# Performance work log

Hardware: AMD Instinct MI355X
Metric: run time of the kernel (lower is better)

The kernel has to match this reference:

```python
import jax, jax.numpy as jnp
import numpy as np

N = 50000          # nodes
E = 800000         # edges (avg in-degree 16)
NFEAT, F = 128, 64 # input feat, hidden width (outfeat = outd_1 = outd_2 = 64)
ALPHA = 0.2        # leaky relu slope
AVG_LIN = 16.0             # sum(bin*hist)/N for deg histogram (all deg 16)
AVG_LOG = float(np.log(17.0))  # sum(log(bin+1)*hist)/N


def setup_inputs():
    key = jax.random.key(0)
    ks = jax.random.split(key, 16)
    g = lambda i, shp, s: (jax.random.normal(ks[i], shp, jnp.float32) * s)
    return {
        "x": g(0, (N, NFEAT), 1.0),
        "adj": jnp.zeros((1,), jnp.float32),
        "edge_index": jax.random.randint(ks[1], (2, E), 0, N, dtype=jnp.int32),
        "W0": g(2, (NFEAT, F), NFEAT ** -0.5), "b0": jnp.zeros((F,), jnp.float32),
        "c1_pre_W": g(3, (2 * F, F), (2 * F) ** -0.5), "c1_pre_b": jnp.zeros((F,), jnp.float32),
        "c1_post_W": g(4, (5 * F, F), (5 * F) ** -0.5), "c1_post_b": jnp.zeros((F,), jnp.float32),
        "c1_lin_W": g(5, (F, F), F ** -0.5), "c1_lin_b": jnp.zeros((F,), jnp.float32),
        "c2_pre_W": g(6, (2 * F, F), (2 * F) ** -0.5), "c2_pre_b": jnp.zeros((F,), jnp.float32),
        "c2_post_W": g(7, (5 * F, F), (5 * F) ** -0.5), "c2_post_b": jnp.zeros((F,), jnp.float32),
        "c2_lin_W": g(8, (F, F), F ** -0.5), "c2_lin_b": jnp.zeros((F,), jnp.float32),
        "W2": g(9, (F, 1), F ** -0.5), "b2": jnp.zeros((1,), jnp.float32),
    }


def pna_conv(x, src, dst, pre_W, pre_b, post_W, post_b, lin_W, lin_b):
    # message: pre_nn(cat[x_i, x_j]) per edge  (x_i = target, x_j = source)
    h = jnp.concatenate([x[dst], x[src]], axis=-1) @ pre_W + pre_b  # [E, F]
    cnt = jax.ops.segment_sum(jnp.ones((h.shape[0],), h.dtype), dst, num_segments=N)
    deg = jnp.clip(cnt, 1.0)                                        # [N]
    mean = jax.ops.segment_sum(h, dst, num_segments=N) / deg[:, None]
    mx = jax.ops.segment_max(h, dst, num_segments=N)
    mx = jnp.where(cnt[:, None] > 0, mx, 0.0)                       # empty segs -> 0
    agg = jnp.concatenate([mean, mx], axis=-1)                      # [N, 2F]
    att = agg * (AVG_LOG / jnp.log(deg + 1.0))[:, None]             # attenuation scaler
    lin = agg * (deg / AVG_LIN)[:, None]                            # linear scaler
    out = jnp.concatenate([x, att, lin], axis=-1)                   # [N, 5F]
    out = out @ post_W + post_b
    return out @ lin_W + lin_b


def reference(x, adj, edge_index, W0, b0,
              c1_pre_W, c1_pre_b, c1_post_W, c1_post_b, c1_lin_W, c1_lin_b,
              c2_pre_W, c2_pre_b, c2_post_W, c2_post_b, c2_lin_W, c2_lin_b,
              W2, b2):
    src, dst = edge_index[0], edge_index[1]
    h = jax.nn.leaky_relu(x @ W0 + b0, negative_slope=ALPHA)  # dropout = id (eval)
    h = jax.nn.relu(pna_conv(h, src, dst, c1_pre_W, c1_pre_b, c1_post_W, c1_post_b, c1_lin_W, c1_lin_b))
    h = jax.nn.relu(pna_conv(h, src, dst, c2_pre_W, c2_pre_b, c2_post_W, c2_post_b, c2_lin_W, c2_lin_b))
    return h @ W2 + b2  # [N, 1]
```

## Files before the change

### kernel.cpp

```cpp
#include <hip/hip_runtime.h>
#include <hip/hip_bf16.h>

typedef __hip_bfloat16 bf16;
typedef unsigned short u16;
typedef unsigned int u32;
typedef __attribute__((ext_vector_type(8))) short short8;
typedef __attribute__((ext_vector_type(4))) float f32x4;

static constexpr float AVG_LOG_C = 2.8332133440562162f;
#define BCAP 1024
#define CHUNK 4096
#define PREP_TOTAL (8192 * 3 + 20480 * 2 + 64 * 6 + 1)

__device__ __forceinline__ u32 f2bf_bits(float f) {
    u32 u = __float_as_uint(f);
    return (u + 0x7fffu + ((u >> 16) & 1u)) >> 16;
}
__device__ __forceinline__ float bf2f(u16 b) {
    return __uint_as_float(((u32)b) << 16);
}

__global__ __launch_bounds__(1024) void detect_zero_kernel(
    const u32* __restrict__ xwords, int* __restrict__ flag,
    int* __restrict__ bcnt, int nb) {
    if (blockIdx.x == 0) {
        int tid = threadIdx.x;
        if (tid < 64) {
            int good = 0;
            for (int i = tid; i < 2048; i += 64) {
                u32 lo = xwords[i] & 0xffffu;
                float v = __uint_as_float(lo << 16);
                float a = fabsf(v);
                if (v == 0.0f || (a >= 1e-3f && a <= 100.0f)) good++;
            }
            for (int off = 32; off; off >>= 1) good += __shfl_xor(good, off, 64);
            if (tid == 0) *flag = (2 * good > 2048) ? 1 : 0;
        }
    } else {
        int i = (blockIdx.x - 1) * 1024 + threadIdx.x;
        if (i < nb) bcnt[i] = 0;
    }
}

__global__ __launch_bounds__(1024) void prep_scatter_kernel(
    const int* __restrict__ srcs, const int* __restrict__ dsts,
    int* __restrict__ bcnt, u32* __restrict__ bstage, int e, int nb,
    const void* __restrict__ W0r,  const void* __restrict__ b0r,
    const void* __restrict__ pre1r, const void* __restrict__ preb1r,
    const void* __restrict__ post1r, const void* __restrict__ postb1r,
    const void* __restrict__ lin1r, const void* __restrict__ linb1r,
    const void* __restrict__ pre2r, const void* __restrict__ preb2r,
    const void* __restrict__ post2r, const void* __restrict__ postb2r,
    const void* __restrict__ lin2r, const void* __restrict__ linb2r,
    const void* __restrict__ W2r,  const void* __restrict__ b2r,
    u16* __restrict__ W0p, u16* __restrict__ pre1p, u16* __restrict__ pre2p,
    u16* __restrict__ wf1p, u16* __restrict__ wf2p,
    float* __restrict__ bfo1, float* __restrict__ bfo2,
    float* __restrict__ preb1f, float* __restrict__ preb2f,
    float* __restrict__ b0f, float* __restrict__ W2f, float* __restrict__ b2f,
    const int* __restrict__ flag) {
    __shared__ int lhist[2048];
    __shared__ int lbase[2048];
    int tid = threadIdx.x;
    int scatB = (e + CHUNK - 1) / CHUNK;
    if ((int)blockIdx.x < scatB) {
        int cbase = blockIdx.x * CHUNK;
        for (int b = tid; b < nb; b += 1024) lhist[b] = 0;
        __syncthreads();
#pragma unroll
        for (int i = 0; i < CHUNK; i += 1024) {
            int e0 = cbase + i + tid;
            if (e0 < e) atomicAdd(&lhist[dsts[e0] >> 5], 1);
        }
        __syncthreads();
        for (int b = tid; b < nb; b += 1024) {
            int c = lhist[b];
            lbase[b] = c ? atomicAdd(&bcnt[b], c) : 0;
            lhist[b] = 0;
        }
        __syncthreads();
#pragma unroll
        for (int i = 0; i < CHUNK; i += 1024) {
            int e0 = cbase + i + tid;
            if (e0 < e) {
                int d = dsts[e0];
                int b = d >> 5;
                int pos = lbase[b] + atomicAdd(&lhist[b], 1);
                if (pos < BCAP)
                    bstage[(size_t)b * BCAP + pos] = (u32)srcs[e0] | ((u32)(d & 31) << 17);
            }
        }
        return;
    }
    int idx = ((int)blockIdx.x - scatB) * 1024 + tid;
    bool isbf = (*flag) != 0;
    auto ld = [&](const void* p, int i) -> float {
        return isbf ? bf2f(((const u16*)p)[i]) : ((const float*)p)[i];
    };
    if (idx < 8192) {
        int j = idx & 7, l = (idx >> 3) & 63, tt = idx >> 9;
        int c = tt & 3, s = tt >> 2;
        int kk = s * 32 + (l >> 4) * 8 + j;
        int col = c * 16 + (l & 15);
        W0p[idx] = (u16)f2bf_bits(ld(W0r, kk * 64 + col));
        return;
    }
    idx -= 8192;
    for (int which = 0; which < 2; ++which) {
        if (idx < 8192) {
            const void* src = which ? pre2r : pre1r;
            u16* dst = which ? pre2p : pre1p;
            int j = idx & 7, l = (idx >> 3) & 63, tt = idx >> 9;
            int c = tt & 7, s = tt >> 3;
            int kk = s * 32 + (l >> 4) * 8 + j;
            int col = c * 16 + (l & 15);
            float v = (col < 64) ? ld(src, kk * 64 + col)
                                 : ld(src, (64 + kk) * 64 + (col - 64));
            dst[idx] = (u16)f2bf_bits(v);
            return;
        }
        idx -= 8192;
    }
    for (int which = 0; which < 2; ++which) {
        if (idx < 20480) {
            const void* postW = which ? post2r : post1r;
            const void* linW  = which ? lin2r  : lin1r;
            u16* dst = which ? wf2p : wf1p;
            int j = idx & 7, l = (idx >> 3) & 63, tt = idx >> 9;
            int c = tt & 3, s = tt >> 2;
            int kk = s * 32 + (l >> 4) * 8 + j;
            int col = c * 16 + (l & 15);
            float a = 0.f;
            for (int k = 0; k < 64; ++k)
                a = fmaf(ld(postW, kk * 64 + k), ld(linW, k * 64 + col), a);
            dst[idx] = (u16)f2bf_bits(a);
            return;
        }
        idx -= 20480;
    }
    for (int which = 0; which < 2; ++which) {
        if (idx < 64) {
            const void* postb = which ? postb2r : postb1r;
            const void* linW  = which ? lin2r : lin1r;
            const void* linb  = which ? linb2r : linb1r;
            float* dst = which ? bfo2 : bfo1;
            float a = ld(linb, idx);
            for (int k = 0; k < 64; ++k)
                a = fmaf(ld(postb, k), ld(linW, k * 64 + idx), a);
            dst[idx] = a;
            return;
        }
        idx -= 64;
    }
    if (idx < 64) { preb1f[idx] = ld(preb1r, idx); return; }
    idx -= 64;
    if (idx < 64) { preb2f[idx] = ld(preb2r, idx); return; }
    idx -= 64;
    if (idx < 64) { b0f[idx] = ld(b0r, idx); return; }
    idx -= 64;
    if (idx < 64) { W2f[idx] = ld(W2r, idx); return; }
    idx -= 64;
    if (idx < 1) { b2f[0] = ld(b2r, 0); }
}

__global__ __launch_bounds__(512, 6) void gemm_x_pq_kernel(
    const void* __restrict__ xraw, const u16* __restrict__ W0p,
    const float* __restrict__ b0f, const u16* __restrict__ pre1p,
    u16* __restrict__ hA, u16* __restrict__ PQ,
    const int* __restrict__ flag, int n) {
    __shared__ __align__(16) u16 xsh[32 * 136];
    __shared__ __align__(16) u16 hsh[32 * 72];
    int tid = threadIdx.x;
    int wave = __builtin_amdgcn_readfirstlane(tid >> 6);
    int lane = tid & 63;
    int blockbase = blockIdx.x * 32;
    bool isbf = (*flag) != 0;
    {
        int row = tid >> 4;
        int cg = (tid & 15) * 8;
        int grow = blockbase + row;
        short8 v = short8{0, 0, 0, 0, 0, 0, 0, 0};
        if (grow < n) {
            if (isbf) {
                v = *(const short8*)((const u16*)xraw + (size_t)grow * 128 + cg);
            } else {
                const float* xf = (const float*)xraw + (size_t)grow * 128 + cg;
                f32x4 a0 = *(const f32x4*)xf;
                f32x4 a1 = *(const f32x4*)(xf + 4);
#pragma unroll
                for (int j = 0; j < 4; ++j) {
                    v[j]     = (short)f2bf_bits(a0[j]);
                    v[4 + j] = (short)f2bf_bits(a1[j]);
                }
            }
        }
        *(short8*)&xsh[row * 136 + cg] = v;
    }
    __syncthreads();
    int rt = wave & 1, ct = wave >> 1;
    int arl = rt * 16 + (lane & 15);
    int koff = (lane >> 4) * 8;
    f32x4 acc = f32x4{0.f, 0.f, 0.f, 0.f};
#pragma unroll
    for (int s = 0; s < 4; ++s) {
        short8 a = *(const short8*)&xsh[arl * 136 + s * 32 + koff];
        short8 b = *(const short8*)(W0p + ((size_t)(s * 4 + ct) * 64 + lane) * 8);
        acc = __builtin_amdgcn_mfma_f32_16x16x32_bf16(a, b, acc, 0, 0, 0);
    }
    {
        int col = ct * 16 + (lane & 15);
        float bv = b0f[col];
        int r0l = rt * 16 + (lane >> 4) * 4;
#pragma unroll
        for (int r = 0; r < 4; ++r) {
            float v = acc[r] + bv;
            v = v > 0.f ? v : 0.2f * v;
            u16 bits = (u16)f2bf_bits(v);
            hsh[(r0l + r) * 72 + col] = bits;
            int grow = blockbase + r0l + r;
            if (grow < n) hA[(size_t)grow * 64 + col] = bits;
        }
    }
    __syncthreads();
#pragma unroll
    for (int half = 0; half < 2; ++half) {
        int tile = wave * 2 + half;
        int rt2 = tile & 1, ct2 = tile >> 1;
        int ar2 = rt2 * 16 + (lane & 15);
        f32x4 acc2 = f32x4{0.f, 0.f, 0.f, 0.f};
#pragma unroll
        for (int s = 0; s < 2; ++s) {
            short8 a = *(const short8*)&hsh[ar2 * 72 + s * 32 + koff];
            short8 b = *(const short8*)(pre1p + ((size_t)(s * 8 + ct2) * 64 + lane) * 8);
            acc2 = __builtin_amdgcn_mfma_f32_16x16x32_bf16(a, b, acc2, 0, 0, 0);
        }
        int col2 = ct2 * 16 + (lane & 15);
        int r02 = rt2 * 16 + (lane >> 4) * 4;
#pragma unroll
        for (int r = 0; r < 4; ++r) {
            int grow = blockbase + r02 + r;
            if (grow < n) PQ[(size_t)grow * 128 + col2] = (u16)f2bf_bits(acc2[r]);
        }
    }
}

template<int FINAL>
__global__ __launch_bounds__(512, 6) void agg_gemm_kernel(
    const u16* __restrict__ PQ, const u16* __restrict__ h,
    const u32* __restrict__ bstage, const int* __restrict__ bcnt,
    const float* __restrict__ prebf, const u16* __restrict__ Wfp,
    const float* __restrict__ bfo, const u16* __restrict__ prenextp,
    u16* __restrict__ hout, u16* __restrict__ PQout,
    const float* __restrict__ W2f, const float* __restrict__ b2f,
    void* __restrict__ out, const int* __restrict__ flag, int n) {
    constexpr int PAD = 328;
    __shared__ __align__(16) u16 vsh[32 * PAD];
    __shared__ __align__(16) u16 hsh[32 * 72];
    __shared__ u32 lel[BCAP];
    __shared__ int loff[32], lcnt[32], lcur[32];
    __shared__ float fsum[32];
    int tid = threadIdx.x;
    int wave = __builtin_amdgcn_readfirstlane(tid >> 6);
    int lane = tid & 63;
    int b = blockIdx.x;
    int blockbase = b * 32;
    float pbl = prebf[lane];
    if (tid < 32) { lcnt[tid] = 0; if (FINAL) fsum[tid] = 0.f; }
    __syncthreads();
    int cb = min(bcnt[b], BCAP);
    const u32* st = bstage + (size_t)b * BCAP;
    for (int i = tid; i < cb; i += 512) atomicAdd(&lcnt[st[i] >> 17], 1);
    __syncthreads();
    if (wave == 0) {
        int c = (lane < 32) ? lcnt[lane] : 0;
        int s = c;
        for (int off = 1; off < 32; off <<= 1) {
            int t = __shfl_up(s, (unsigned)off, 64);
            if (lane >= off) s += t;
        }
        if (lane < 32) {
            loff[lane] = s - c;
            lcur[lane] = s - c;
        }
    }
    __syncthreads();
    for (int i = tid; i < cb; i += 512) {
        u32 e = st[i];
        int pos = atomicAdd(&lcur[e >> 17], 1);
        lel[pos] = (e & 0x1ffffu) << 8;
    }
    __syncthreads();
    const char* PQc = (const char*)PQ;
    u32 voffb = 128u + 2u * (u32)lane;
#pragma unroll
    for (int t = 0; t < 4; ++t) {
        int nl = wave * 4 + t;
        int node = blockbase + nl;
        u16* vrow = &vsh[nl * PAD];
        if (node < n) {
            int beg = loff[nl], end = beg + lcnt[nl];
            int cnt = end - beg;
            float s = 0.f, m = -3.4e38f;
            int e = beg;
            for (; e + 8 <= end; e += 8) {
                float q0 = bf2f(*(const u16*)(PQc + lel[e]     + voffb));
                float q1 = bf2f(*(const u16*)(PQc + lel[e + 1] + voffb));
                float q2 = bf2f(*(const u16*)(PQc + lel[e + 2] + voffb));
                float q3 = bf2f(*(const u16*)(PQc + lel[e + 3] + voffb));
                float q4 = bf2f(*(const u16*)(PQc + lel[e + 4] + voffb));
                float q5 = bf2f(*(const u16*)(PQc + lel[e + 5] + voffb));
                float q6 = bf2f(*(const u16*)(PQc + lel[e + 6] + voffb));
                float q7 = bf2f(*(const u16*)(PQc + lel[e + 7] + voffb));
                s += ((q0 + q1) + (q2 + q3)) + ((q4 + q5) + (q6 + q7));
                m = fmaxf(m, fmaxf(fmaxf(fmaxf(q0, q1), fmaxf(q2, q3)),
                                   fmaxf(fmaxf(q4, q5), fmaxf(q6, q7))));
            }
            for (; e + 4 <= end; e += 4) {
                float q0 = bf2f(*(const u16*)(PQc + lel[e]     + voffb));
                float q1 = bf2f(*(const u16*)(PQc + lel[e + 1] + voffb));
                float q2 = bf2f(*(const u16*)(PQc + lel[e + 2] + voffb));
                float q3 = bf2f(*(const u16*)(PQc + lel[e + 3] + voffb));
                s += (q0 + q1) + (q2 + q3);
                m = fmaxf(fmaxf(m, fmaxf(q0, q1)), fmaxf(q2, q3));
            }
            for (; e < end; ++e) {
                float q = bf2f(*(const u16*)(PQc + lel[e] + voffb));
                s += q;
                m = fmaxf(m, q);
            }
            float mean, mx, deg;
            if (cnt > 0) {
                deg = (float)cnt;
                float p = bf2f(PQ[(size_t)node * 128 + lane]) + pbl;
                mean = p + s / deg;
                mx = p + m;
            } else {
                deg = 1.f; mean = 0.f; mx = 0.f;
            }
            float att = AVG_LOG_C / logf(deg + 1.f);
            float lin = deg * (1.f / 16.f);
            vrow[lane]       = h[(size_t)node * 64 + lane];
            vrow[64 + lane]  = (u16)f2bf_bits(att * mean);
            vrow[128 + lane] = (u16)f2bf_bits(att * mx);
            vrow[192 + lane] = (u16)f2bf_bits(lin * mean);
            vrow[256 + lane] = (u16)f2bf_bits(lin * mx);
        } else {
            vrow[lane] = 0; vrow[64 + lane] = 0; vrow[128 + lane] = 0;
            vrow[192 + lane] = 0; vrow[256 + lane] = 0;
        }
    }
    __syncthreads();
    int rt = wave & 1, ct = wave >> 1;
    int arl = rt * 16 + (lane & 15);
    int koff = (lane >> 4) * 8;
    f32x4 acc = f32x4{0.f, 0.f, 0.f, 0.f};
#pragma unroll
    for (int s = 0; s < 10; ++s) {
        short8 a = *(const short8*)&vsh[arl * PAD + s * 32 + koff];
        short8 b2 = *(const short8*)(Wfp + ((size_t)(s * 4 + ct) * 64 + lane) * 8);
        acc = __builtin_amdgcn_mfma_f32_16x16x32_bf16(a, b2, acc, 0, 0, 0);
    }
    int col = ct * 16 + (lane & 15);
    float bv = bfo[col];
    int r0l = rt * 16 + (lane >> 4) * 4;
    if constexpr (!FINAL) {
#pragma unroll
        for (int r = 0; r < 4; ++r) {
            float v = fmaxf(acc[r] + bv, 0.f);
            u16 bits = (u16)f2bf_bits(v);
            hsh[(r0l + r) * 72 + col] = bits;
            int grow = blockbase + r0l + r;
            if (grow < n) hout[(size_t)grow * 64 + col] = bits;
        }
        __syncthreads();
#pragma unroll
        for (int half = 0; half < 2; ++half) {
            int tile = wave * 2 + half;
            int rt2 = tile & 1, ct2 = tile >> 1;
            int ar2 = rt2 * 16 + (lane & 15);
            f32x4 acc2 = f32x4{0.f, 0.f, 0.f, 0.f};
#pragma unroll
            for (int s = 0; s < 2; ++s) {
                short8 a = *(const short8*)&hsh[ar2 * 72 + s * 32 + koff];
                short8 b2 = *(const short8*)(prenextp + ((size_t)(s * 8 + ct2) * 64 + lane) * 8);
                acc2 = __builtin_amdgcn_mfma_f32_16x16x32_bf16(a, b2, acc2, 0, 0, 0);
            }
            int col2 = ct2 * 16 + (lane & 15);
            int r02 = rt2 * 16 + (lane >> 4) * 4;
#pragma unroll
            for (int r = 0; r < 4; ++r) {
                int grow = blockbase + r02 + r;
                if (grow < n) PQout[(size_t)grow * 128 + col2] = (u16)f2bf_bits(acc2[r]);
            }
        }
    } else {
        float w2 = W2f[col];
        float part[4];
#pragma unroll
        for (int r = 0; r < 4; ++r)
            part[r] = fmaxf(acc[r] + bv, 0.f) * w2;
#pragma unroll
        for (int r = 0; r < 4; ++r) {
            float v = part[r];
            v += __shfl_xor(v, 1, 64);
            v += __shfl_xor(v, 2, 64);
            v += __shfl_xor(v, 4, 64);
            v += __shfl_xor(v, 8, 64);
            if ((lane & 15) == 0) atomicAdd(&fsum[r0l + r], v);
        }
        __syncthreads();
        if (tid < 32) {
            int grow = blockbase + tid;
            if (grow < n) {
                float res = fsum[tid] + b2f[0];
                if (*flag) ((u16*)out)[grow] = (u16)f2bf_bits(res);
                else       ((float*)out)[grow] = res;
            }
        }
    }
}

extern "C" void kernel_launch(void* const* d_in, const int* in_sizes, int n_in,
                              void* d_out, int out_size, void* d_ws, size_t ws_size,
                              hipStream_t stream) {
    const int N = in_sizes[0] / 128;
    const int E = in_sizes[2] / 2;
    const int nb = (N + 31) >> 5;
    const int* ei = (const int*)d_in[2];
    const int* esrc = ei;
    const int* edst = ei + E;

    char* w = (char*)d_ws;
    auto alloc = [&](size_t bytes) -> void* {
        void* p = (void*)w;
        w += (bytes + 255) & ~(size_t)255;
        return p;
    };
    int* flag    = (int*)alloc(4);
    int* bcnt    = (int*)alloc((size_t)nb * 4);
    u32* bstage  = (u32*)alloc((size_t)nb * BCAP * 4);
    u16* W0p     = (u16*)alloc(128 * 64 * 2);
    u16* pre1p   = (u16*)alloc(64 * 128 * 2);
    u16* pre2p   = (u16*)alloc(64 * 128 * 2);
    u16* wf1p    = (u16*)alloc(320 * 64 * 2);
    u16* wf2p    = (u16*)alloc(320 * 64 * 2);
    float* bfo1  = (float*)alloc(64 * 4);
    float* bfo2  = (float*)alloc(64 * 4);
    float* preb1f= (float*)alloc(64 * 4);
    float* preb2f= (float*)alloc(64 * 4);
    float* b0f   = (float*)alloc(64 * 4);
    float* W2f   = (float*)alloc(64 * 4);
    float* b2f_  = (float*)alloc(4);
    u16* hA      = (u16*)alloc((size_t)N * 64 * 2);
    u16* hB      = (u16*)alloc((size_t)N * 64 * 2);
    u16* PQA     = (u16*)alloc((size_t)N * 128 * 2);
    u16* PQB     = (u16*)alloc((size_t)N * 128 * 2);

    detect_zero_kernel<<<1 + (nb + 1023) / 1024, 1024, 0, stream>>>(
        (const u32*)d_in[0], flag, bcnt, nb);

    int scatB = (E + CHUNK - 1) / CHUNK;
    int prepB = (PREP_TOTAL + 1023) / 1024;
    prep_scatter_kernel<<<scatB + prepB, 1024, 0, stream>>>(
        esrc, edst, bcnt, bstage, E, nb,
        d_in[3], d_in[4], d_in[5], d_in[6], d_in[7], d_in[8], d_in[9], d_in[10],
        d_in[11], d_in[12], d_in[13], d_in[14], d_in[15], d_in[16], d_in[17], d_in[18],
        W0p, pre1p, pre2p, wf1p, wf2p,
        bfo1, bfo2, preb1f, preb2f, b0f, W2f, b2f_, flag);

    int gblocks = (N + 31) / 32;
    gemm_x_pq_kernel<<<gblocks, 512, 0, stream>>>(
        d_in[0], W0p, b0f, pre1p, hA, PQA, flag, N);

    agg_gemm_kernel<0><<<gblocks, 512, 0, stream>>>(
        PQA, hA, bstage, bcnt, preb1f, wf1p, bfo1, pre2p, hB, PQB,
        nullptr, nullptr, nullptr, flag, N);

    agg_gemm_kernel<1><<<gblocks, 512, 0, stream>>>(
        PQB, hB, bstage, bcnt, preb2f, wf2p, bfo2, nullptr, nullptr, nullptr,
        W2f, b2f_, d_out, flag, N);
}
```

Baseline: 204.6 us.

## Merge input GEMM, edge scatter and weight prep into one kernel launch

Folds the first GEMM (x@W0 then pre1 projection) into the same launch as the edge bucket scatter and weight packing. Each GEMM block reads raw weights directly and detects the input dtype itself, so it no longer waits on a separate flag kernel or on packed W0/pre1 buffers. The bcnt zeroing moves to a memset, the scatter chunk shrinks to suit 512-thread blocks, and agg occupancy hints drop from 6 to 4. The aim is fewer launches and serial dependencies. The cost is redundant dtype detection in every block and uncoalesced strided weight loads inside the GEMM.

```diff
diff --git a/kernel.cpp b/kernel.cpp
--- a/kernel.cpp
+++ b/kernel.cpp
@@ -9,8 +9,8 @@
 
 static constexpr float AVG_LOG_C = 2.8332133440562162f;
 #define BCAP 1024
-#define CHUNK 4096
-#define PREP_TOTAL (8192 * 3 + 20480 * 2 + 64 * 6 + 1)
+#define CHUNK 2048
+#define PREP_TOTAL (8192 + 20480 * 2 + 64 * 5 + 1)
 
 __device__ __forceinline__ u32 f2bf_bits(float f) {
     u32 u = __float_as_uint(f);
@@ -20,31 +20,42 @@
     return __uint_as_float(((u32)b) << 16);
 }
 
-__global__ __launch_bounds__(1024) void detect_zero_kernel(
-    const u32* __restrict__ xwords, int* __restrict__ flag,
-    int* __restrict__ bcnt, int nb) {
-    if (blockIdx.x == 0) {
-        int tid = threadIdx.x;
-        if (tid < 64) {
-            int good = 0;
-            for (int i = tid; i < 2048; i += 64) {
-                u32 lo = xwords[i] & 0xffffu;
-                float v = __uint_as_float(lo << 16);
-                float a = fabsf(v);
-                if (v == 0.0f || (a >= 1e-3f && a <= 100.0f)) good++;
-            }
-            for (int off = 32; off; off >>= 1) good += __shfl_xor(good, off, 64);
-            if (tid == 0) *flag = (2 * good > 2048) ? 1 : 0;
-        }
+__device__ __forceinline__ bool block_detect(const u32* __restrict__ xwords,
+                                             int* sflag, int tid) {
+    if (tid < 64) {
+        int good = 0;
+        for (int i = tid; i < 2048; i += 64) {
+            u32 lo = xwords[i] & 0xffffu;
+            float v = __uint_as_float(lo << 16);
+            float a = fabsf(v);
+            if (v == 0.0f || (a >= 1e-3f && a <= 100.0f)) good++;
+        }
+        for (int off = 32; off; off >>= 1) good += __shfl_xor(good, off, 64);
+        if (tid == 0) *sflag = (2 * good > 2048) ? 1 : 0;
+    }
+    __syncthreads();
+    return *sflag != 0;
+}
+
+__device__ __forceinline__ short8 load_bfrag_raw(const void* __restrict__ W, bool isbf,
+                                                 int kk0, int col) {
+    short8 r;
+    if (isbf) {
+        const u16* p = (const u16*)W + (size_t)kk0 * 64 + col;
+#pragma unroll
+        for (int j = 0; j < 8; ++j) r[j] = (short)p[j * 64];
     } else {
-        int i = (blockIdx.x - 1) * 1024 + threadIdx.x;
-        if (i < nb) bcnt[i] = 0;
-    }
-}
-
-__global__ __launch_bounds__(1024) void prep_scatter_kernel(
+        const float* p = (const float*)W + (size_t)kk0 * 64 + col;
+#pragma unroll
+        for (int j = 0; j < 8; ++j) r[j] = (short)f2bf_bits(p[j * 64]);
+    }
+    return r;
+}
+
+__global__ __launch_bounds__(512, 4) void k1_kernel(
+    const void* __restrict__ xraw,
     const int* __restrict__ srcs, const int* __restrict__ dsts,
-    int* __restrict__ bcnt, u32* __restrict__ bstage, int e, int nb,
+    int* __restrict__ bcnt, u32* __restrict__ bstage,
     const void* __restrict__ W0r,  const void* __restrict__ b0r,
     const void* __restrict__ pre1r, const void* __restrict__ preb1r,
     const void* __restrict__ post1r, const void* __restrict__ postb1r,
@@ -53,74 +64,145 @@
     const void* __restrict__ post2r, const void* __restrict__ postb2r,
     const void* __restrict__ lin2r, const void* __restrict__ linb2r,
     const void* __restrict__ W2r,  const void* __restrict__ b2r,
-    u16* __restrict__ W0p, u16* __restrict__ pre1p, u16* __restrict__ pre2p,
-    u16* __restrict__ wf1p, u16* __restrict__ wf2p,
+    u16* __restrict__ pre2p, u16* __restrict__ wf1p, u16* __restrict__ wf2p,
     float* __restrict__ bfo1, float* __restrict__ bfo2,
     float* __restrict__ preb1f, float* __restrict__ preb2f,
-    float* __restrict__ b0f, float* __restrict__ W2f, float* __restrict__ b2f,
-    const int* __restrict__ flag) {
-    __shared__ int lhist[2048];
-    __shared__ int lbase[2048];
+    float* __restrict__ W2f, float* __restrict__ b2f, int* __restrict__ flag,
+    u16* __restrict__ hA, u16* __restrict__ PQ,
+    int n, int e, int nb, int gB, int scatB) {
+    __shared__ union {
+        struct { int lhist[2048]; int lbase[2048]; } sc;
+        struct { __align__(16) u16 xsh[32 * 136]; __align__(16) u16 hsh[32 * 72]; } gx;
+    } sm;
+    __shared__ int sflag;
     int tid = threadIdx.x;
-    int scatB = (e + CHUNK - 1) / CHUNK;
-    if ((int)blockIdx.x < scatB) {
-        int cbase = blockIdx.x * CHUNK;
-        for (int b = tid; b < nb; b += 1024) lhist[b] = 0;
-        __syncthreads();
-#pragma unroll
-        for (int i = 0; i < CHUNK; i += 1024) {
+    int bx = (int)blockIdx.x;
+
+    if (bx < gB) {
+        int wave = __builtin_amdgcn_readfirstlane(tid >> 6);
+        int lane = tid & 63;
+        int blockbase = bx * 32;
+        bool isbf = block_detect((const u32*)xraw, &sflag, tid);
+        {
+            int row = tid >> 4;
+            int cgx = (tid & 15) * 8;
+            int grow = blockbase + row;
+            short8 v = short8{0, 0, 0, 0, 0, 0, 0, 0};
+            if (grow < n) {
+                if (isbf) {
+                    v = *(const short8*)((const u16*)xraw + (size_t)grow * 128 + cgx);
+                } else {
+                    const float* xf = (const float*)xraw + (size_t)grow * 128 + cgx;
+                    f32x4 a0 = *(const f32x4*)xf;
+                    f32x4 a1 = *(const f32x4*)(xf + 4);
+#pragma unroll
+                    for (int j = 0; j < 4; ++j) {
+                        v[j]     = (short)f2bf_bits(a0[j]);
+                        v[4 + j] = (short)f2bf_bits(a1[j]);
+                    }
+                }
+            }
+            *(short8*)&sm.gx.xsh[row * 136 + cgx] = v;
+        }
+        __syncthreads();
+        int rt = wave & 1, ct = wave >> 1;
+        int arl = rt * 16 + (lane & 15);
+        int koff = (lane >> 4) * 8;
+        int colh = ct * 16 + (lane & 15);
+        f32x4 acc = f32x4{0.f, 0.f, 0.f, 0.f};
+#pragma unroll
+        for (int s = 0; s < 4; ++s) {
+            short8 a = *(const short8*)&sm.gx.xsh[arl * 136 + s * 32 + koff];
+            short8 b = load_bfrag_raw(W0r, isbf, s * 32 + (lane >> 4) * 8, colh);
+            acc = __builtin_amdgcn_mfma_f32_16x16x32_bf16(a, b, acc, 0, 0, 0);
+        }
+        {
+            float bv = isbf ? bf2f(((const u16*)b0r)[colh]) : ((const float*)b0r)[colh];
+            int r0l = rt * 16 + (lane >> 4) * 4;
+#pragma unroll
+            for (int r = 0; r < 4; ++r) {
+                float v = acc[r] + bv;
+                v = v > 0.f ? v : 0.2f * v;
+                u16 bits = (u16)f2bf_bits(v);
+                sm.gx.hsh[(r0l + r) * 72 + colh] = bits;
+                int grow = blockbase + r0l + r;
+                if (grow < n) hA[(size_t)grow * 64 + colh] = bits;
+            }
+        }
+        __syncthreads();
+#pragma unroll
+        for (int half = 0; half < 2; ++half) {
+            int tile = wave * 2 + half;
+            int rt2 = tile & 1, ct2 = tile >> 1;
+            int ar2 = rt2 * 16 + (lane & 15);
+            int col128 = ct2 * 16 + (lane & 15);
+            int colw = col128 & 63;
+            int radd = (col128 < 64) ? 0 : 64;
+            f32x4 acc2 = f32x4{0.f, 0.f, 0.f, 0.f};
+#pragma unroll
+            for (int s = 0; s < 2; ++s) {
+                short8 a = *(const short8*)&sm.gx.hsh[ar2 * 72 + s * 32 + koff];
+                short8 b = load_bfrag_raw(pre1r, isbf,
+                                          s * 32 + (lane >> 4) * 8 + radd, colw);
+                acc2 = __builtin_amdgcn_mfma_f32_16x16x32_bf16(a, b, acc2, 0, 0, 0);
+            }
+            int r02 = rt2 * 16 + (lane >> 4) * 4;
+#pragma unroll
+            for (int r = 0; r < 4; ++r) {
+                int grow = blockbase + r02 + r;
+                if (grow < n) PQ[(size_t)grow * 128 + col128] = (u16)f2bf_bits(acc2[r]);
+            }
+        }
+        return;
+    }
+
+    if (bx < gB + scatB) {
+        int cbase = (bx - gB) * CHUNK;
+        for (int bb = tid; bb < nb; bb += 512) sm.sc.lhist[bb] = 0;
+        __syncthreads();
+#pragma unroll
+        for (int i = 0; i < CHUNK; i += 512) {
             int e0 = cbase + i + tid;
-            if (e0 < e) atomicAdd(&lhist[dsts[e0] >> 5], 1);
-        }
-        __syncthreads();
-        for (int b = tid; b < nb; b += 1024) {
-            int c = lhist[b];
-            lbase[b] = c ? atomicAdd(&bcnt[b], c) : 0;
-            lhist[b] = 0;
-        }
-        __syncthreads();
-#pragma unroll
-        for (int i = 0; i < CHUNK; i += 1024) {
+            if (e0 < e) atomicAdd(&sm.sc.lhist[dsts[e0] >> 5], 1);
+        }
+        __syncthreads();
+        for (int bb = tid; bb < nb; bb += 512) {
+            int c = sm.sc.lhist[bb];
+            sm.sc.lbase[bb] = c ? atomicAdd(&bcnt[bb], c) : 0;
+            sm.sc.lhist[bb] = 0;
+        }
+        __syncthreads();
+#pragma unroll
+        for (int i = 0; i < CHUNK; i += 512) {
             int e0 = cbase + i + tid;
             if (e0 < e) {
                 int d = dsts[e0];
-                int b = d >> 5;
-                int pos = lbase[b] + atomicAdd(&lhist[b], 1);
+                int bb = d >> 5;
+                int pos = sm.sc.lbase[bb] + atomicAdd(&sm.sc.lhist[bb], 1);
                 if (pos < BCAP)
-                    bstage[(size_t)b * BCAP + pos] = (u32)srcs[e0] | ((u32)(d & 31) << 17);
+                    bstage[(size_t)bb * BCAP + pos] = (u32)srcs[e0] | ((u32)(d & 31) << 17);
             }
         }
         return;
     }
-    int idx = ((int)blockIdx.x - scatB) * 1024 + tid;
-    bool isbf = (*flag) != 0;
+
+    bool isbf = block_detect((const u32*)xraw, &sflag, tid);
+    if (bx == gB + scatB && tid == 0) *flag = sflag;
     auto ld = [&](const void* p, int i) -> float {
         return isbf ? bf2f(((const u16*)p)[i]) : ((const float*)p)[i];
     };
+    int idx = (bx - gB - scatB) * 512 + tid;
     if (idx < 8192) {
         int j = idx & 7, l = (idx >> 3) & 63, tt = idx >> 9;
-        int c = tt & 3, s = tt >> 2;
+        int c = tt & 7, s = tt >> 3;
         int kk = s * 32 + (l >> 4) * 8 + j;
         int col = c * 16 + (l & 15);
-        W0p[idx] = (u16)f2bf_bits(ld(W0r, kk * 64 + col));
+        float v = (col < 64) ? ld(pre2r, kk * 64 + col)
+                             : ld(pre2r, (64 + kk) * 64 + (col - 64));
+        pre2p[idx] = (u16)f2bf_bits(v);
         return;
     }
     idx -= 8192;
-    for (int which = 0; which < 2; ++which) {
-        if (idx < 8192) {
-            const void* src = which ? pre2r : pre1r;
-            u16* dst = which ? pre2p : pre1p;
-            int j = idx & 7, l = (idx >> 3) & 63, tt = idx >> 9;
-            int c = tt & 7, s = tt >> 3;
-            int kk = s * 32 + (l >> 4) * 8 + j;
-            int col = c * 16 + (l & 15);
-            float v = (col < 64) ? ld(src, kk * 64 + col)
-                                 : ld(src, (64 + kk) * 64 + (col - 64));
-            dst[idx] = (u16)f2bf_bits(v);
-            return;
-        }
-        idx -= 8192;
-    }
     for (int which = 0; which < 2; ++which) {
         if (idx < 20480) {
             const void* postW = which ? post2r : post1r;
@@ -156,96 +238,13 @@
     idx -= 64;
     if (idx < 64) { preb2f[idx] = ld(preb2r, idx); return; }
     idx -= 64;
-    if (idx < 64) { b0f[idx] = ld(b0r, idx); return; }
-    idx -= 64;
     if (idx < 64) { W2f[idx] = ld(W2r, idx); return; }
     idx -= 64;
     if (idx < 1) { b2f[0] = ld(b2r, 0); }
 }
 
-__global__ __launch_bounds__(512, 6) void gemm_x_pq_kernel(
-    const void* __restrict__ xraw, const u16* __restrict__ W0p,
-    const float* __restrict__ b0f, const u16* __restrict__ pre1p,
-    u16* __restrict__ hA, u16* __restrict__ PQ,
-    const int* __restrict__ flag, int n) {
-    __shared__ __align__(16) u16 xsh[32 * 136];
-    __shared__ __align__(16) u16 hsh[32 * 72];
-    int tid = threadIdx.x;
-    int wave = __builtin_amdgcn_readfirstlane(tid >> 6);
-    int lane = tid & 63;
-    int blockbase = blockIdx.x * 32;
-    bool isbf = (*flag) != 0;
-    {
-        int row = tid >> 4;
-        int cg = (tid & 15) * 8;
-        int grow = blockbase + row;
-        short8 v = short8{0, 0, 0, 0, 0, 0, 0, 0};
-        if (grow < n) {
-            if (isbf) {
-                v = *(const short8*)((const u16*)xraw + (size_t)grow * 128 + cg);
-            } else {
-                const float* xf = (const float*)xraw + (size_t)grow * 128 + cg;
-                f32x4 a0 = *(const f32x4*)xf;
-                f32x4 a1 = *(const f32x4*)(xf + 4);
-#pragma unroll
-                for (int j = 0; j < 4; ++j) {
-                    v[j]     = (short)f2bf_bits(a0[j]);
-                    v[4 + j] = (short)f2bf_bits(a1[j]);
-                }
-            }
-        }
-        *(short8*)&xsh[row * 136 + cg] = v;
-    }
-    __syncthreads();
-    int rt = wave & 1, ct = wave >> 1;
-    int arl = rt * 16 + (lane & 15);
-    int koff = (lane >> 4) * 8;
-    f32x4 acc = f32x4{0.f, 0.f, 0.f, 0.f};
-#pragma unroll
-    for (int s = 0; s < 4; ++s) {
-        short8 a = *(const short8*)&xsh[arl * 136 + s * 32 + koff];
-        short8 b = *(const short8*)(W0p + ((size_t)(s * 4 + ct) * 64 + lane) * 8);
-        acc = __builtin_amdgcn_mfma_f32_16x16x32_bf16(a, b, acc, 0, 0, 0);
-    }
-    {
-        int col = ct * 16 + (lane & 15);
-        float bv = b0f[col];
-        int r0l = rt * 16 + (lane >> 4) * 4;
-#pragma unroll
-        for (int r = 0; r < 4; ++r) {
-            float v = acc[r] + bv;
-            v = v > 0.f ? v : 0.2f * v;
-            u16 bits = (u16)f2bf_bits(v);
-            hsh[(r0l + r) * 72 + col] = bits;
-            int grow = blockbase + r0l + r;
-            if (grow < n) hA[(size_t)grow * 64 + col] = bits;
-        }
-    }
-    __syncthreads();
-#pragma unroll
-    for (int half = 0; half < 2; ++half) {
-        int tile = wave * 2 + half;
-        int rt2 = tile & 1, ct2 = tile >> 1;
-        int ar2 = rt2 * 16 + (lane & 15);
-        f32x4 acc2 = f32x4{0.f, 0.f, 0.f, 0.f};
-#pragma unroll
-        for (int s = 0; s < 2; ++s) {
-            short8 a = *(const short8*)&hsh[ar2 * 72 + s * 32 + koff];
-            short8 b = *(const short8*)(pre1p + ((size_t)(s * 8 + ct2) * 64 + lane) * 8);
-            acc2 = __builtin_amdgcn_mfma_f32_16x16x32_bf16(a, b, acc2, 0, 0, 0);
-        }
-        int col2 = ct2 * 16 + (lane & 15);
-        int r02 = rt2 * 16 + (lane >> 4) * 4;
-#pragma unroll
-        for (int r = 0; r < 4; ++r) {
-            int grow = blockbase + r02 + r;
-            if (grow < n) PQ[(size_t)grow * 128 + col2] = (u16)f2bf_bits(acc2[r]);
-        }
-    }
-}
-
 template<int FINAL>
-__global__ __launch_bounds__(512, 6) void agg_gemm_kernel(
+__global__ __launch_bounds__(512, 4) void agg_gemm_kernel(
     const u16* __restrict__ PQ, const u16* __restrict__ h,
     const u32* __restrict__ bstage, const int* __restrict__ bcnt,
     const float* __restrict__ prebf, const u16* __restrict__ Wfp,
@@ -439,8 +438,6 @@
     int* flag    = (int*)alloc(4);
     int* bcnt    = (int*)alloc((size_t)nb * 4);
     u32* bstage  = (u32*)alloc((size_t)nb * BCAP * 4);
-    u16* W0p     = (u16*)alloc(128 * 64 * 2);
-    u16* pre1p   = (u16*)alloc(64 * 128 * 2);
     u16* pre2p   = (u16*)alloc(64 * 128 * 2);
     u16* wf1p    = (u16*)alloc(320 * 64 * 2);
     u16* wf2p    = (u16*)alloc(320 * 64 * 2);
@@ -448,7 +445,6 @@
     float* bfo2  = (float*)alloc(64 * 4);
     float* preb1f= (float*)alloc(64 * 4);
     float* preb2f= (float*)alloc(64 * 4);
-    float* b0f   = (float*)alloc(64 * 4);
     float* W2f   = (float*)alloc(64 * 4);
     float* b2f_  = (float*)alloc(4);
     u16* hA      = (u16*)alloc((size_t)N * 64 * 2);
@@ -456,27 +452,23 @@
     u16* PQA     = (u16*)alloc((size_t)N * 128 * 2);
     u16* PQB     = (u16*)alloc((size_t)N * 128 * 2);
 
-    detect_zero_kernel<<<1 + (nb + 1023) / 1024, 1024, 0, stream>>>(
-        (const u32*)d_in[0], flag, bcnt, nb);
-
+    hipMemsetAsync(bcnt, 0, (size_t)nb * 4, stream);
+
+    int gB = (N + 31) / 32;
     int scatB = (E + CHUNK - 1) / CHUNK;
-    int prepB = (PREP_TOTAL + 1023) / 1024;
-    prep_scatter_kernel<<<scatB + prepB, 1024, 0, stream>>>(
-        esrc, edst, bcnt, bstage, E, nb,
+    int prepB = (PREP_TOTAL + 511) / 512;
+    k1_kernel<<<gB + scatB + prepB, 512, 0, stream>>>(
+        d_in[0], esrc, edst, bcnt, bstage,
         d_in[3], d_in[4], d_in[5], d_in[6], d_in[7], d_in[8], d_in[9], d_in[10],
         d_in[11], d_in[12], d_in[13], d_in[14], d_in[15], d_in[16], d_in[17], d_in[18],
-        W0p, pre1p, pre2p, wf1p, wf2p,
-        bfo1, bfo2, preb1f, preb2f, b0f, W2f, b2f_, flag);
-
-    int gblocks = (N + 31) / 32;
-    gemm_x_pq_kernel<<<gblocks, 512, 0, stream>>>(
-        d_in[0], W0p, b0f, pre1p, hA, PQA, flag, N);
-
-    agg_gemm_kernel<0><<<gblocks, 512, 0, stream>>>(
+        pre2p, wf1p, wf2p, bfo1, bfo2, preb1f, preb2f, W2f, b2f_, flag,
+        hA, PQA, N, E, nb, gB, scatB);
+
+    agg_gemm_kernel<0><<<gB, 512, 0, stream>>>(
         PQA, hA, bstage, bcnt, preb1f, wf1p, bfo1, pre2p, hB, PQB,
         nullptr, nullptr, nullptr, flag, N);
 
-    agg_gemm_kernel<1><<<gblocks, 512, 0, stream>>>(
+    agg_gemm_kernel<1><<<gB, 512, 0, stream>>>(
         PQB, hB, bstage, bcnt, preb2f, wf2p, bfo2, nullptr, nullptr, nullptr,
         W2f, b2f_, d_out, flag, N);
 }
```

Result: no change. 206.4 us (+0.9%).
